# Performance work log

Hardware: AMD Instinct MI355X
Metric: run time of the kernel (lower is better)

Reference implementation:

```python
import jax, jax.numpy as jnp
import numpy as np

B, S, H, NH, L = 8, 768, 768, 12, 12
W = 128          # one-sided window = attention_window // 2 (chunk_size=256)
D = H // NH      # head dim = 64
FF = 4 * H
EPS = 1e-12      # LongformerConfig layer_norm_eps
MAX_POS = 1024


def setup_inputs() -> dict:
    key = jax.random.key(0)
    ks = iter(jax.random.split(key, 64))
    rn = lambda shape, s=0.02: jax.random.normal(next(ks), shape, jnp.float32) * s
    inp = {
        "embedding": jax.random.normal(next(ks), (B, S, H), jnp.float32),
        "mask": jnp.ones((B, S), jnp.int32),  # unused by the original forward's core call
        "pos_emb": rn((MAX_POS, H)),
        "tte": rn((H,)),  # token_type embedding row 0 (token_type_ids are all zero)
        "emb_ln_g": jnp.ones((H,), jnp.float32),
        "emb_ln_b": jnp.zeros((H,), jnp.float32),
        "Wq": rn((L, H, H)), "bq": jnp.zeros((L, H), jnp.float32),
        "Wk": rn((L, H, H)), "bk": jnp.zeros((L, H), jnp.float32),
        "Wv": rn((L, H, H)), "bv": jnp.zeros((L, H), jnp.float32),
        "Wo": rn((L, H, H)), "bo": jnp.zeros((L, H), jnp.float32),
        "ln1_g": jnp.ones((L, H), jnp.float32), "ln1_b": jnp.zeros((L, H), jnp.float32),
        "Wi": rn((L, H, FF)), "bi": jnp.zeros((L, FF), jnp.float32),
        "Wo2": rn((L, FF, H)), "bo2": jnp.zeros((L, H), jnp.float32),
        "ln2_g": jnp.ones((L, H), jnp.float32), "ln2_b": jnp.zeros((L, H), jnp.float32),
        "gate_w": rn((H,)), "gate_b": jnp.zeros((), jnp.float32),
    }
    return inp


def layer_norm(x, g, b):
    mu = jnp.mean(x, axis=-1, keepdims=True)
    var = jnp.mean(jnp.square(x - mu), axis=-1, keepdims=True)
    return (x - mu) * jax.lax.rsqrt(var + EPS) * g + b


def sliding_window_attention(q, k, v):
    # q,k,v: [B,S,H]; each query attends to keys within +-W positions (band of 2W+1).
    n = S // W
    split = lambda x: x.reshape(B, S, NH, D).transpose(0, 2, 1, 3)  # [B,NH,S,D]
    qh = split(q) / np.sqrt(D)
    kh, vh = split(k), split(v)
    qc = qh.reshape(B, NH, n, W, D)

    def chunk3(x):
        # pad one chunk of zeros each side, gather [prev, cur, next] key chunks
        xp = jnp.pad(x, ((0, 0), (0, 0), (W, W), (0, 0))).reshape(B, NH, n + 2, W, D)
        return jnp.concatenate([xp[:, :, i:i + n] for i in range(3)], axis=3)  # [B,NH,n,3W,D]

    k3, v3 = chunk3(kh), chunk3(vh)
    scores = jnp.einsum('bhnqd,bhnkd->bhnqk', qc, k3)  # [B,NH,n,W,3W]

    qi = jnp.arange(W)[:, None]
    kj = jnp.arange(3 * W)[None, :]
    rel = kj - W - qi                                   # relative position j - i
    jglob = (jnp.arange(n)[:, None, None] - 1) * W + kj  # absolute key position
    valid = (jnp.abs(rel) <= W) & (jglob >= 0) & (jglob < S)  # [n,W,3W]

    scores = jnp.where(valid, scores, -1e9)
    p = jax.nn.softmax(scores, axis=-1)
    out = jnp.einsum('bhnqk,bhnkd->bhnqd', p, v3)
    return out.reshape(B, NH, S, D).transpose(0, 2, 1, 3).reshape(B, S, H)


def reference(embedding, mask, pos_emb, tte, emb_ln_g, emb_ln_b,
              Wq, bq, Wk, bk, Wv, bv, Wo, bo, ln1_g, ln1_b,
              Wi, bi, Wo2, bo2, ln2_g, ln2_b, gate_w, gate_b):
    # embeddings (position ids start at padding_idx+1 = 2, RoBERTa-style)
    pos_ids = jnp.arange(S) + 2
    x = embedding + pos_emb[pos_ids] + tte
    x = layer_norm(x, emb_ln_g, emb_ln_b)

    def layer(h, p):
        wq, b_q, wk, b_k, wv, b_v, wo, b_o, g1, be1, wi, b_i, wo2, b_o2, g2, be2 = p
        q = h @ wq + b_q
        k = h @ wk + b_k
        v = h @ wv + b_v
        a = sliding_window_attention(q, k, v)
        h = layer_norm(h + a @ wo + b_o, g1, be1)
        ff = jax.nn.gelu(h @ wi + b_i, approximate=False)
        h = layer_norm(h + ff @ wo2 + b_o2, g2, be2)
        return h, None

    x, _ = jax.lax.scan(layer, x, (Wq, bq, Wk, bk, Wv, bv, Wo, bo, ln1_g, ln1_b,
                                   Wi, bi, Wo2, bo2, ln2_g, ln2_b))
    gate = x @ gate_w + gate_b  # [B,S]
    return x, gate
```

## Files before the change

### kernel.cpp

```cpp
#include <hip/hip_runtime.h>
#include <hip/hip_bf16.h>
#include <math.h>
#include <stdint.h>

typedef __hip_bfloat16 bf16;
typedef __attribute__((ext_vector_type(8))) __bf16 bf16x8;
typedef __attribute__((ext_vector_type(4))) float f32x4;

#define HDIM 768
#define MROWS 6144
#define NCHUNK 6

__device__ __forceinline__ float bf2f(unsigned int u) {
  union { unsigned int i; float f; } c; c.i = u << 16; return c.f;
}

__device__ __forceinline__ void gload16(const void* g, void* l) {
  __builtin_amdgcn_global_load_lds((const __attribute__((address_space(1))) void*)g,
                                   (__attribute__((address_space(3))) void*)l, 16, 0, 0);
}

__device__ __forceinline__ float gelu_f(float v) {
  const float u2 = 1.5957691216057308f * (v + 0.044715f * v * v * v);
  const float e = __expf(u2);
  const float th = 1.f - 2.f / (e + 1.f);
  return 0.5f * v * (1.f + th);
}

__global__ __launch_bounds__(256) void wconv(
    const float* __restrict__ Wq, const float* __restrict__ Wk,
    const float* __restrict__ Wv, const float* __restrict__ Wo,
    const float* __restrict__ Wi, const float* __restrict__ Wo2,
    bf16* __restrict__ wt)
{
  __shared__ float tile[32][33];
  const int bid = blockIdx.x;
  const float* src; bf16* dst; int K, N, tIdx;
  if (bid < 2304) {
    int m = bid / 576; tIdx = bid % 576; K = 768; N = 768;
    src = (m == 0) ? Wq : (m == 1) ? Wk : (m == 2) ? Wv : Wo;
    dst = wt + (size_t)m * 589824;
  } else if (bid < 4608) {
    tIdx = bid - 2304; K = 768; N = 3072; src = Wi; dst = wt + 2359296;
  } else {
    tIdx = bid - 4608; K = 3072; N = 768; src = Wo2; dst = wt + 4718592;
  }
  const int tilesN = N >> 5;
  const int tn = tIdx % tilesN, tk = tIdx / tilesN;
  const int n0 = tn * 32, k0 = tk * 32;
  const int tx = threadIdx.x & 31, ty = threadIdx.x >> 5;
#pragma unroll
  for (int r = 0; r < 4; ++r)
    tile[ty + r * 8][tx] = src[(size_t)(k0 + ty + r * 8) * N + n0 + tx];
  __syncthreads();
#pragma unroll
  for (int r = 0; r < 4; ++r)
    dst[(size_t)(n0 + ty + r * 8) * K + k0 + tx] = __float2bfloat16(tile[tx][ty + r * 8]);
}

__global__ __launch_bounds__(256, 3) void gemm128(
    const bf16* __restrict__ A, const bf16* __restrict__ Bt,
    void* __restrict__ out, const float* __restrict__ b0,
    const float* __restrict__ b1, const float* __restrict__ b2,
    int gx, int N, int K, int NT, int epi)
{
  __shared__ __align__(16) bf16 As[3][4096];
  __shared__ __align__(16) bf16 Bs[3][4096];

  const int nwg = gridDim.x;
  const int wg = blockIdx.x;
  const int L = (wg & 7) * (nwg >> 3) + (wg >> 3);
  const int bx = L % gx, by = L / gx;
  const int m0 = by * 128, n0 = bx * 128;

  const int t = threadIdx.x;
  const int lane = t & 63;
  const int w = t >> 6;
  const int wr = w >> 1, wc = w & 1;
  const int fr = lane & 15;
  const int g = lane >> 4;

  f32x4 acc[4][4];
#pragma unroll
  for (int i = 0; i < 4; ++i)
#pragma unroll
    for (int j = 0; j < 4; ++j) acc[i][j] = (f32x4)0.f;

  const int r0 = t >> 2, q0 = t & 3;
  const int sq = q0 ^ ((r0 >> 1) & 3);
  const bf16* gA0 = A + (size_t)(m0 + r0) * K + sq * 8;
  const bf16* gB0 = Bt + (size_t)(n0 + r0) * K + sq * 8;
  const int dst0 = t * 16;

  unsigned offA[4], offB[4];
#pragma unroll
  for (int mf = 0; mf < 4; ++mf) {
    const int R = wr * 64 + mf * 16 + fr;
    offA[mf] = (unsigned)((R * 64 + g * 16) ^ (((R >> 1) & 3) << 4));
  }
#pragma unroll
  for (int nf = 0; nf < 4; ++nf) {
    const int R = wc * 64 + nf * 16 + fr;
    offB[nf] = (unsigned)((R * 64 + g * 16) ^ (((R >> 1) & 3) << 4));
  }
  const unsigned ldsA = (unsigned)(uintptr_t)&As[0][0];
  const unsigned ldsB = (unsigned)(uintptr_t)&Bs[0][0];

#define STAGE(KT, RB) {                                                    \
    const bf16* a_ = gA0 + (size_t)(KT) * 32;                              \
    const bf16* b_ = gB0 + (size_t)(KT) * 32;                              \
    gload16(a_,                  (char*)As[RB] + dst0);                    \
    gload16(a_ + (size_t)64 * K, (char*)As[RB] + dst0 + 4096);             \
    gload16(b_,                  (char*)Bs[RB] + dst0);                    \
    gload16(b_ + (size_t)64 * K, (char*)Bs[RB] + dst0 + 4096); }

  STAGE(0, 0)
  STAGE(1, 1)

#define ITER(KT, CUR, PFB) {                                               \
    const int pf_ = ((KT) + 2 < NT) ? (KT) + 2 : NT - 1;                   \
    STAGE(pf_, PFB)                                                        \
    asm volatile("s_waitcnt vmcnt(8)" ::: "memory");                       \
    __builtin_amdgcn_s_barrier();                                          \
    bf16x8 af[4], bfr[4];                                                  \
    const unsigned baA_ = ldsA + (CUR) * 8192u;                            \
    const unsigned baB_ = ldsB + (CUR) * 8192u;                            \
    _Pragma("unroll")                                                      \
    for (int mf = 0; mf < 4; ++mf)                                         \
      asm volatile("ds_read_b128 %0, %1" : "=v"(af[mf]) : "v"(baA_ + offA[mf])); \
    _Pragma("unroll")                                                      \
    for (int nf = 0; nf < 4; ++nf)                                         \
      asm volatile("ds_read_b128 %0, %1" : "=v"(bfr[nf]) : "v"(baB_ + offB[nf])); \
    asm volatile("s_waitcnt lgkmcnt(0)" ::: "memory");                     \
    __builtin_amdgcn_sched_barrier(0);                                     \
    __builtin_amdgcn_s_barrier();                                          \
    __builtin_amdgcn_s_setprio(1);                                         \
    _Pragma("unroll")                                                      \
    for (int mf = 0; mf < 4; ++mf)                                         \
      _Pragma("unroll")                                                    \
      for (int nf = 0; nf < 4; ++nf)                                       \
        acc[mf][nf] = __builtin_amdgcn_mfma_f32_16x16x32_bf16(af[mf], bfr[nf], acc[mf][nf], 0, 0, 0); \
    __builtin_amdgcn_s_setprio(0);                                         \
  }

#pragma unroll 1
  for (int kt = 0; kt < NT; kt += 3) {
    ITER(kt, 0, 2)
    ITER(kt + 1, 1, 0)
    ITER(kt + 2, 2, 1)
  }
  asm volatile("s_waitcnt vmcnt(0)" ::: "memory");
#undef ITER
#undef STAGE

  const int rr = (lane >> 4) * 4;
  const int cc0 = lane & 15;
  if (epi == 0) {
    const int mat = n0 / HDIM;
    const float* bias = (mat == 0) ? b0 : (mat == 1) ? b1 : b2;
    const float qs = (mat == 0) ? 0.125f : 1.0f;
    bf16* dst = (bf16*)out + (size_t)mat * MROWS * HDIM;
    const int nl = n0 - mat * HDIM;
#pragma unroll
    for (int mf = 0; mf < 4; ++mf)
#pragma unroll
      for (int nf = 0; nf < 4; ++nf) {
        const int row = m0 + wr * 64 + mf * 16 + rr;
        const int col = nl + wc * 64 + nf * 16 + cc0;
        const float bv = bias[col];
#pragma unroll
        for (int r = 0; r < 4; ++r)
          dst[(size_t)(row + r) * HDIM + col] = __float2bfloat16((acc[mf][nf][r] + bv) * qs);
      }
  } else if (epi == 2) {
    bf16* dst = (bf16*)out;
#pragma unroll
    for (int mf = 0; mf < 4; ++mf)
#pragma unroll
      for (int nf = 0; nf < 4; ++nf) {
        const int row = m0 + wr * 64 + mf * 16 + rr;
        const int col = n0 + wc * 64 + nf * 16 + cc0;
        const float bv = b0[col];
#pragma unroll
        for (int r = 0; r < 4; ++r)
          dst[(size_t)(row + r) * N + col] = __float2bfloat16(gelu_f(acc[mf][nf][r] + bv));
      }
  } else {
    bf16* dst = (bf16*)out;
#pragma unroll
    for (int mf = 0; mf < 4; ++mf)
#pragma unroll
      for (int nf = 0; nf < 4; ++nf) {
        const int row = m0 + wr * 64 + mf * 16 + rr;
        const int col = n0 + wc * 64 + nf * 16 + cc0;
        const float bv = b0[col];
#pragma unroll
        for (int r = 0; r < 4; ++r)
          dst[(size_t)(row + r) * N + col] = __float2bfloat16(acc[mf][nf][r] + bv);
      }
  }
}

__global__ __launch_bounds__(256) void attn_mfma(
    const bf16* __restrict__ qkv, bf16* __restrict__ attb)
{
  const int c = blockIdx.x, h = blockIdx.y, b = blockIdx.z;
  __shared__ unsigned int Vtw[64 * 64];
  __shared__ __align__(16) bf16 Pl[4][32 * 40];
  const int t = threadIdx.x;
  const int lane = t & 63;
  const int w = t >> 6;
  const int fr = lane & 15;
  const int g = lane >> 4;
  const bf16* Km = qkv + (size_t)4718592;
  const bf16* Vm = qkv + (size_t)9437184;
  const size_t qrow0 = (size_t)(b * 768 + c * 128);

  bf16x8 qf[2][2];
#pragma unroll
  for (int nt = 0; nt < 2; ++nt)
#pragma unroll
    for (int ks = 0; ks < 2; ++ks)
      qf[nt][ks] = *(const bf16x8*)(qkv + (qrow0 + w * 32 + nt * 16 + fr) * HDIM + h * 64 + ks * 32 + g * 8);

  f32x4 oacc[4][2];
#pragma unroll
  for (int i = 0; i < 4; ++i) { oacc[i][0] = (f32x4)0.f; oacc[i][1] = (f32x4)0.f; }
  float mrun[2] = {-1e30f, -1e30f};
  float lrun[2] = {0.f, 0.f};

#pragma unroll 1
  for (int cc = c - 1; cc <= c + 1; ++cc) {
    if (cc < 0 || cc >= NCHUNK) continue;
    __syncthreads();
    {
      const int d0 = (t & 7) * 8;
#pragma unroll
      for (int half = 0; half < 2; ++half) {
        const int kp2 = (t >> 3) + half * 32;
        const bf16* vr = Vm + ((size_t)(b * 768 + cc * 128) + kp2 * 2) * HDIM + h * 64 + d0;
        uint4 r0 = *(const uint4*)vr;
        uint4 r1 = *(const uint4*)(vr + HDIM);
        unsigned int a0[4] = {r0.x, r0.y, r0.z, r0.w};
        unsigned int a1[4] = {r1.x, r1.y, r1.z, r1.w};
#pragma unroll
        for (int e = 0; e < 8; ++e) {
          const int d = d0 + e;
          unsigned int lo = (a0[e >> 1] >> ((e & 1) * 16)) & 0xffffu;
          unsigned int hi = (a1[e >> 1] >> ((e & 1) * 16)) & 0xffffu;
          unsigned int byteoff = (unsigned int)(d * 256 + kp2 * 4);
          byteoff ^= ((((d >> 3) ^ d) & 7) << 4);
          Vtw[byteoff >> 2] = lo | (hi << 16);
        }
      }
    }
    __syncthreads();
    const int mode = (cc < c) ? 0 : (cc == c ? 1 : 2);
    const bf16* Kc = Km + ((size_t)(b * 768 + cc * 128)) * HDIM + h * 64;

#pragma unroll 1
    for (int kb = 0; kb < 4; ++kb) {
      f32x4 sacc[2][2];
      sacc[0][0] = sacc[0][1] = sacc[1][0] = sacc[1][1] = (f32x4)0.f;
#pragma unroll
      for (int ks = 0; ks < 2; ++ks)
#pragma unroll
        for (int mt = 0; mt < 2; ++mt) {
          bf16x8 kf = *(const bf16x8*)(Kc + (size_t)(kb * 32 + mt * 16 + fr) * HDIM + ks * 32 + g * 8);
          sacc[mt][0] = __builtin_amdgcn_mfma_f32_16x16x32_bf16(kf, qf[0][ks], sacc[mt][0], 0, 0, 0);
          sacc[mt][1] = __builtin_amdgcn_mfma_f32_16x16x32_bf16(kf, qf[1][ks], sacc[mt][1], 0, 0, 0);
        }
#pragma unroll
      for (int nt = 0; nt < 2; ++nt) {
        const int iq = w * 32 + nt * 16 + fr;
        float pm = -1e30f;
#pragma unroll
        for (int mt = 0; mt < 2; ++mt)
#pragma unroll
          for (int r = 0; r < 4; ++r) {
            const int j = kb * 32 + mt * 16 + g * 4 + r;
            const bool valid = (mode == 1) || (mode == 0 ? (j >= iq) : (j <= iq));
            const float sv = valid ? sacc[mt][nt][r] : -1e30f;
            sacc[mt][nt][r] = sv;
            pm = fmaxf(pm, sv);
          }
        pm = fmaxf(pm, __shfl_xor(pm, 16));
        pm = fmaxf(pm, __shfl_xor(pm, 32));
        const float mnew = fmaxf(fmaxf(mrun[nt], pm), -1e20f);
        const float sc = __expf(mrun[nt] - mnew);
        mrun[nt] = mnew;
        lrun[nt] *= sc;
#pragma unroll
        for (int mt = 0; mt < 4; ++mt) oacc[mt][nt] *= sc;
        float ps = 0.f;
#pragma unroll
        for (int mt = 0; mt < 2; ++mt) {
          union { bf16 hh[4]; uint2 uu; } pk;
#pragma unroll
          for (int r = 0; r < 4; ++r) {
            const float p = __expf(sacc[mt][nt][r] - mnew);
            ps += p;
            pk.hh[r] = __float2bfloat16(p);
          }
          *(uint2*)(&Pl[w][(nt * 16 + fr) * 40 + mt * 16 + g * 4]) = pk.uu;
        }
        ps += __shfl_xor(ps, 16);
        ps += __shfl_xor(ps, 32);
        lrun[nt] += ps;
      }
      bf16x8 bpf[2];
#pragma unroll
      for (int nt = 0; nt < 2; ++nt)
        bpf[nt] = *(const bf16x8*)(&Pl[w][(nt * 16 + fr) * 40 + g * 8]);
#pragma unroll
      for (int mt = 0; mt < 4; ++mt) {
        const int d = mt * 16 + fr;
        unsigned int byteoff = (unsigned int)(d * 256 + kb * 64 + g * 16);
        byteoff ^= ((((d >> 3) ^ d) & 7) << 4);
        bf16x8 vf = *(const bf16x8*)((const char*)Vtw + byteoff);
        oacc[mt][0] = __builtin_amdgcn_mfma_f32_16x16x32_bf16(vf, bpf[0], oacc[mt][0], 0, 0, 0);
        oacc[mt][1] = __builtin_amdgcn_mfma_f32_16x16x32_bf16(vf, bpf[1], oacc[mt][1], 0, 0, 0);
      }
    }
  }
#pragma unroll
  for (int nt = 0; nt < 2; ++nt) {
    const float rl = 1.f / lrun[nt];
    bf16* orow = attb + (qrow0 + w * 32 + nt * 16 + fr) * HDIM + h * 64;
#pragma unroll
    for (int mt = 0; mt < 4; ++mt) {
      union { bf16 hh[4]; uint2 uu; } ok;
#pragma unroll
      for (int r = 0; r < 4; ++r) ok.hh[r] = __float2bfloat16(oacc[mt][nt][r] * rl);
      *(uint2*)(orow + mt * 16 + g * 4) = ok.uu;
    }
  }
}

__device__ __forceinline__ void blk_reduce2(float& s1, float& s2) {
#pragma unroll
  for (int o = 32; o > 0; o >>= 1) { s1 += __shfl_xor(s1, o); s2 += __shfl_xor(s2, o); }
  __shared__ float red[8];
  const int w = threadIdx.x >> 6;
  if ((threadIdx.x & 63) == 0) { red[w] = s1; red[4 + w] = s2; }
  __syncthreads();
  s1 = red[0] + red[1] + red[2] + red[3];
  s2 = red[4] + red[5] + red[6] + red[7];
}

__global__ __launch_bounds__(256) void embed_ln(
    const float* __restrict__ emb, const float* __restrict__ pos,
    const float* __restrict__ tte, const float* __restrict__ g,
    const float* __restrict__ bt, float* __restrict__ x, bf16* __restrict__ xb)
{
  const int row = blockIdx.x;
  const int s = row % 768;
  const int t = threadIdx.x;
  const size_t base = (size_t)row * HDIM;
  const size_t pbase = (size_t)(s + 2) * HDIM;
  float v[3];
#pragma unroll
  for (int i = 0; i < 3; ++i) {
    const int idx = t + i * 256;
    v[i] = emb[base + idx] + pos[pbase + idx] + tte[idx];
  }
  float s1 = v[0] + v[1] + v[2];
  float s2 = v[0]*v[0] + v[1]*v[1] + v[2]*v[2];
  blk_reduce2(s1, s2);
  const float mu = s1 * (1.f / 768.f);
  const float var = s2 * (1.f / 768.f) - mu * mu;
  const float inv = rsqrtf(var + 1e-12f);
#pragma unroll
  for (int i = 0; i < 3; ++i) {
    const int idx = t + i * 256;
    const float o = (v[i] - mu) * inv * g[idx] + bt[idx];
    x[base + idx] = o;
    xb[base + idx] = __float2bfloat16(o);
  }
}

__global__ __launch_bounds__(256) void add_ln(
    const bf16* __restrict__ tmp, float* __restrict__ x, bf16* __restrict__ xb,
    const float* __restrict__ g, const float* __restrict__ bt)
{
  const int row = blockIdx.x;
  const int t = threadIdx.x;
  const size_t base = (size_t)row * HDIM;
  float v[3];
#pragma unroll
  for (int i = 0; i < 3; ++i) {
    const int idx = t + i * 256;
    v[i] = x[base + idx] + __bfloat162float(tmp[base + idx]);
  }
  float s1 = v[0] + v[1] + v[2];
  float s2 = v[0]*v[0] + v[1]*v[1] + v[2]*v[2];
  blk_reduce2(s1, s2);
  const float mu = s1 * (1.f / 768.f);
  const float var = s2 * (1.f / 768.f) - mu * mu;
  const float inv = rsqrtf(var + 1e-12f);
#pragma unroll
  for (int i = 0; i < 3; ++i) {
    const int idx = t + i * 256;
    const float o = (v[i] - mu) * inv * g[idx] + bt[idx];
    x[base + idx] = o;
    xb[base + idx] = __float2bfloat16(o);
  }
}

__global__ __launch_bounds__(256) void gate_kernel(
    const float* __restrict__ x, const float* __restrict__ gw,
    const float* __restrict__ gb, float* __restrict__ out)
{
  const int row = blockIdx.x * 4 + (threadIdx.x >> 6);
  const int lane = threadIdx.x & 63;
  const float* xr = x + (size_t)row * HDIM;
  float s = 0.f;
#pragma unroll
  for (int i = 0; i < 12; ++i) s += xr[lane + i * 64] * gw[lane + i * 64];
#pragma unroll
  for (int o = 32; o > 0; o >>= 1) s += __shfl_xor(s, o);
  if (lane == 0) out[row] = s + gb[0];
}

extern "C" void kernel_launch(void* const* d_in, const int* in_sizes, int n_in,
                              void* d_out, int out_size, void* d_ws, size_t ws_size,
                              hipStream_t stream)
{
  const float* emb = (const float*)d_in[0];
  const float* pos = (const float*)d_in[2];
  const float* tte = (const float*)d_in[3];
  const float* eg  = (const float*)d_in[4];
  const float* eb  = (const float*)d_in[5];
  const float* Wq  = (const float*)d_in[6];
  const float* bq  = (const float*)d_in[7];
  const float* Wk  = (const float*)d_in[8];
  const float* bk  = (const float*)d_in[9];
  const float* Wv  = (const float*)d_in[10];
  const float* bv  = (const float*)d_in[11];
  const float* Wo  = (const float*)d_in[12];
  const float* bo  = (const float*)d_in[13];
  const float* g1  = (const float*)d_in[14];
  const float* be1 = (const float*)d_in[15];
  const float* Wi  = (const float*)d_in[16];
  const float* bi  = (const float*)d_in[17];
  const float* Wo2 = (const float*)d_in[18];
  const float* bo2 = (const float*)d_in[19];
  const float* g2  = (const float*)d_in[20];
  const float* be2 = (const float*)d_in[21];
  const float* gw  = (const float*)d_in[22];
  const float* gb  = (const float*)d_in[23];

  char* wsp = (char*)d_ws;
  bf16* wt   = (bf16*)wsp;
  bf16* xb   = (bf16*)(wsp + 14155776);
  bf16* qkvb = (bf16*)(wsp + 23592960);
  bf16* tmp  = (bf16*)(wsp + 61341696);
  bf16* attb = qkvb + (size_t)3 * 4718592;
  bf16* ffb  = qkvb;
  float* x   = (float*)d_out;
  float* gate = x + 4718592;

  embed_ln<<<6144, 256, 0, stream>>>(emb, pos, tte, eg, eb, x, xb);

  for (int l = 0; l < 12; ++l) {
    wconv<<<6912, 256, 0, stream>>>(Wq + (size_t)l * 589824, Wk + (size_t)l * 589824,
                                    Wv + (size_t)l * 589824, Wo + (size_t)l * 589824,
                                    Wi + (size_t)l * 2359296, Wo2 + (size_t)l * 2359296, wt);
    gemm128<<<864, 256, 0, stream>>>(xb, wt, qkvb,
        bq + l * 768, bk + l * 768, bv + l * 768, 18, 2304, 768, 24, 0);
    attn_mfma<<<dim3(6, 12, 8), 256, 0, stream>>>(qkvb, attb);
    gemm128<<<288, 256, 0, stream>>>(attb, wt + 1769472, tmp,
        bo + l * 768, nullptr, nullptr, 6, 768, 768, 24, 3);
    add_ln<<<6144, 256, 0, stream>>>(tmp, x, xb, g1 + l * 768, be1 + l * 768);
    gemm128<<<1152, 256, 0, stream>>>(xb, wt + 2359296, ffb,
        bi + l * 3072, nullptr, nullptr, 24, 3072, 768, 24, 2);
    gemm128<<<288, 256, 0, stream>>>(ffb, wt + 4718592, tmp,
        bo2 + l * 768, nullptr, nullptr, 6, 768, 3072, 96, 3);
    add_ln<<<6144, 256, 0, stream>>>(tmp, x, xb, g2 + l * 768, be2 + l * 768);
  }

  gate_kernel<<<1536, 256, 0, stream>>>(x, gw, gb, gate);
}
```

Measured before the change: 2.760 ms.

## Split-K the FFN down-projection GEMM and double-buffer GEMM LDS for occupancy

The K=3072 down-projection GEMM is split into two K slices, each writing a separate bf16 partial to its own buffer, and a new add_ln2 kernel sums both partials with the residual before layer norm. This doubles the grid from 288 to 576 workgroups so more CUs have work. The GEMM pipeline also moves from triple to double buffering in LDS and raises the launch-bounds occupancy hint from 3 to 5. That leaves less prefetch depth for every GEMM, and rounding each partial to bf16 before the sum adds a little precision loss.

```diff
diff --git a/kernel.cpp b/kernel.cpp
--- a/kernel.cpp
+++ b/kernel.cpp
@@ -58,20 +58,24 @@
     dst[(size_t)(n0 + ty + r * 8) * K + k0 + tx] = __float2bfloat16(tile[tx][ty + r * 8]);
 }
 
-__global__ __launch_bounds__(256, 3) void gemm128(
+__global__ __launch_bounds__(256, 5) void gemm128(
     const bf16* __restrict__ A, const bf16* __restrict__ Bt,
     void* __restrict__ out, const float* __restrict__ b0,
     const float* __restrict__ b1, const float* __restrict__ b2,
-    int gx, int N, int K, int NT, int epi)
-{
-  __shared__ __align__(16) bf16 As[3][4096];
-  __shared__ __align__(16) bf16 Bs[3][4096];
+    int gx, int N, int K, int NT, int epi, int nslice)
+{
+  __shared__ __align__(16) bf16 As[2][4096];
+  __shared__ __align__(16) bf16 Bs[2][4096];
 
   const int nwg = gridDim.x;
   const int wg = blockIdx.x;
   const int L = (wg & 7) * (nwg >> 3) + (wg >> 3);
-  const int bx = L % gx, by = L / gx;
+  const int per = nwg / nslice;
+  const int slice = L / per;
+  const int Lr = L - slice * per;
+  const int bx = Lr % gx, by = Lr / gx;
   const int m0 = by * 128, n0 = bx * 128;
+  const int kb0 = slice * (NT << 5);
 
   const int t = threadIdx.x;
   const int lane = t & 63;
@@ -88,8 +92,8 @@
 
   const int r0 = t >> 2, q0 = t & 3;
   const int sq = q0 ^ ((r0 >> 1) & 3);
-  const bf16* gA0 = A + (size_t)(m0 + r0) * K + sq * 8;
-  const bf16* gB0 = Bt + (size_t)(n0 + r0) * K + sq * 8;
+  const bf16* gA0 = A + (size_t)(m0 + r0) * K + kb0 + sq * 8;
+  const bf16* gB0 = Bt + (size_t)(n0 + r0) * K + kb0 + sq * 8;
   const int dst0 = t * 16;
 
   unsigned offA[4], offB[4];
@@ -115,12 +119,11 @@
     gload16(b_ + (size_t)64 * K, (char*)Bs[RB] + dst0 + 4096); }
 
   STAGE(0, 0)
-  STAGE(1, 1)
-
-#define ITER(KT, CUR, PFB) {                                               \
-    const int pf_ = ((KT) + 2 < NT) ? (KT) + 2 : NT - 1;                   \
-    STAGE(pf_, PFB)                                                        \
-    asm volatile("s_waitcnt vmcnt(8)" ::: "memory");                       \
+
+#define ITER(KT, CUR) {                                                    \
+    const int pf_ = ((KT) + 1 < NT) ? (KT) + 1 : (KT);                     \
+    STAGE(pf_, (CUR) ^ 1)                                                  \
+    asm volatile("s_waitcnt vmcnt(4)" ::: "memory");                       \
     __builtin_amdgcn_s_barrier();                                          \
     bf16x8 af[4], bfr[4];                                                  \
     const unsigned baA_ = ldsA + (CUR) * 8192u;                            \
@@ -144,10 +147,9 @@
   }
 
 #pragma unroll 1
-  for (int kt = 0; kt < NT; kt += 3) {
-    ITER(kt, 0, 2)
-    ITER(kt + 1, 1, 0)
-    ITER(kt + 2, 2, 1)
+  for (int kt = 0; kt < NT; kt += 2) {
+    ITER(kt, 0)
+    ITER(kt + 1, 1)
   }
   asm volatile("s_waitcnt vmcnt(0)" ::: "memory");
 #undef ITER
@@ -186,14 +188,14 @@
           dst[(size_t)(row + r) * N + col] = __float2bfloat16(gelu_f(acc[mf][nf][r] + bv));
       }
   } else {
-    bf16* dst = (bf16*)out;
+    bf16* dst = (bf16*)out + (size_t)slice * 4718592;
 #pragma unroll
     for (int mf = 0; mf < 4; ++mf)
 #pragma unroll
       for (int nf = 0; nf < 4; ++nf) {
         const int row = m0 + wr * 64 + mf * 16 + rr;
         const int col = n0 + wc * 64 + nf * 16 + cc0;
-        const float bv = b0[col];
+        const float bv = slice ? 0.f : b0[col];
 #pragma unroll
         for (int r = 0; r < 4; ++r)
           dst[(size_t)(row + r) * N + col] = __float2bfloat16(acc[mf][nf][r] + bv);
@@ -391,6 +393,35 @@
   for (int i = 0; i < 3; ++i) {
     const int idx = t + i * 256;
     v[i] = x[base + idx] + __bfloat162float(tmp[base + idx]);
+  }
+  float s1 = v[0] + v[1] + v[2];
+  float s2 = v[0]*v[0] + v[1]*v[1] + v[2]*v[2];
+  blk_reduce2(s1, s2);
+  const float mu = s1 * (1.f / 768.f);
+  const float var = s2 * (1.f / 768.f) - mu * mu;
+  const float inv = rsqrtf(var + 1e-12f);
+#pragma unroll
+  for (int i = 0; i < 3; ++i) {
+    const int idx = t + i * 256;
+    const float o = (v[i] - mu) * inv * g[idx] + bt[idx];
+    x[base + idx] = o;
+    xb[base + idx] = __float2bfloat16(o);
+  }
+}
+
+__global__ __launch_bounds__(256) void add_ln2(
+    const bf16* __restrict__ tmp0, const bf16* __restrict__ tmp1,
+    float* __restrict__ x, bf16* __restrict__ xb,
+    const float* __restrict__ g, const float* __restrict__ bt)
+{
+  const int row = blockIdx.x;
+  const int t = threadIdx.x;
+  const size_t base = (size_t)row * HDIM;
+  float v[3];
+#pragma unroll
+  for (int i = 0; i < 3; ++i) {
+    const int idx = t + i * 256;
+    v[i] = x[base + idx] + __bfloat162float(tmp0[base + idx]) + __bfloat162float(tmp1[base + idx]);
   }
   float s1 = v[0] + v[1] + v[2];
   float s2 = v[0]*v[0] + v[1]*v[1] + v[2]*v[2];
@@ -467,16 +498,16 @@
                                     Wv + (size_t)l * 589824, Wo + (size_t)l * 589824,
                                     Wi + (size_t)l * 2359296, Wo2 + (size_t)l * 2359296, wt);
     gemm128<<<864, 256, 0, stream>>>(xb, wt, qkvb,
-        bq + l * 768, bk + l * 768, bv + l * 768, 18, 2304, 768, 24, 0);
+        bq + l * 768, bk + l * 768, bv + l * 768, 18, 2304, 768, 24, 0, 1);
     attn_mfma<<<dim3(6, 12, 8), 256, 0, stream>>>(qkvb, attb);
     gemm128<<<288, 256, 0, stream>>>(attb, wt + 1769472, tmp,
-        bo + l * 768, nullptr, nullptr, 6, 768, 768, 24, 3);
+        bo + l * 768, nullptr, nullptr, 6, 768, 768, 24, 3, 1);
     add_ln<<<6144, 256, 0, stream>>>(tmp, x, xb, g1 + l * 768, be1 + l * 768);
     gemm128<<<1152, 256, 0, stream>>>(xb, wt + 2359296, ffb,
-        bi + l * 3072, nullptr, nullptr, 24, 3072, 768, 24, 2);
-    gemm128<<<288, 256, 0, stream>>>(ffb, wt + 4718592, tmp,
-        bo2 + l * 768, nullptr, nullptr, 6, 768, 3072, 96, 3);
-    add_ln<<<6144, 256, 0, stream>>>(tmp, x, xb, g2 + l * 768, be2 + l * 768);
+        bi + l * 3072, nullptr, nullptr, 24, 3072, 768, 24, 2, 1);
+    gemm128<<<576, 256, 0, stream>>>(ffb, wt + 4718592, tmp,
+        bo2 + l * 768, nullptr, nullptr, 6, 768, 3072, 48, 3, 2);
+    add_ln2<<<6144, 256, 0, stream>>>(tmp, tmp + 4718592, x, xb, g2 + l * 768, be2 + l * 768);
   }
 
   gate_kernel<<<1536, 256, 0, stream>>>(x, gw, gb, gate);
```

Result: slower. 7.589 ms (+174.9%).
